# Kernel optimization log

Measured on AMD Instinct MI355X. Metric: run time of the kernel, lower is better.

The kernel has to match this reference:

```python
import jax, jax.numpy as jnp
import numpy as np

EPS = 1e-6
SIGMA = 0.02  # inverse-quadratic kernel scale (RGBuvHistBlock default)
H_BINS = 128


def _rgb_uv_hist(x, mu):
    # x: [B, 3, H, W] in [0, 1]; mu: [h] bin centers in [-3, 3]
    x = jnp.clip(x, 0.0, 1.0)
    B = x.shape[0]
    I = x.reshape(B, 3, -1)                       # [B, 3, N]
    Iy = jnp.sqrt(jnp.sum(I * I, axis=1) + EPS)   # [B, N] intensity scaling
    logI = jnp.log(I + EPS)                       # [B, 3, N]

    def kern(d):
        # inverse-quadratic kernel: 1 / (1 + (|d| / sigma)^2)
        return 1.0 / (1.0 + (d / SIGMA) ** 2)

    def chan(c0, c1, c2):
        Iu = logI[:, c0] - logI[:, c1]            # [B, N]
        Iv = logI[:, c0] - logI[:, c2]            # [B, N]
        du = kern(jnp.abs(Iu[:, :, None] - mu[None, None, :]))  # [B, N, h]
        dv = kern(jnp.abs(Iv[:, :, None] - mu[None, None, :]))  # [B, N, h]
        a = Iy[:, :, None] * du                   # [B, N, h]
        return jnp.einsum('bnu,bnv->buv', a, dv)  # [B, h, h]

    # channel order: r vs (g,b), g vs (r,b), b vs (r,g)
    hists = jnp.stack([chan(0, 1, 2), chan(1, 0, 2), chan(2, 0, 1)], axis=1)  # [B,3,h,h]
    norm = jnp.sum(hists, axis=(1, 2, 3)).reshape(-1, 1, 1, 1) + EPS
    return hists / norm


def setup_inputs() -> dict:
    key = jax.random.key(0)
    k1, k2 = jax.random.split(key)
    B, C, H, W = 4, 3, 256, 256
    pred = jax.random.uniform(k1, (B, C, H, W), dtype=jnp.float32)
    target = jax.random.uniform(k2, (B, C, H, W), dtype=jnp.float32)
    return {"pred": pred, "target": target}


def reference(pred, target):
    mu = jnp.linspace(-3.0, 3.0, H_BINS, dtype=pred.dtype)
    pred_hist = _rgb_uv_hist(pred, mu)
    target_hist = _rgb_uv_hist(target, mu)
    diff = jnp.sqrt(target_hist) - jnp.sqrt(pred_hist)
    return (1.0 / np.sqrt(2.0)) * jnp.sqrt(jnp.sum(diff * diff)) / pred_hist.shape[0]
```

## Files before the change

kernel.cpp:

```cpp
#include <hip/hip_runtime.h>

#define NPIX   65536
#define HB     128
#define EPSF   1e-6f
#define ROWB   80
#define MATB   (HB * ROWB)
#define BUFB   (3 * MATB)
#define PPW    24576

typedef _Float16 half8  __attribute__((ext_vector_type(8)));
typedef __fp16   fp16x2 __attribute__((ext_vector_type(2)));
typedef float    f32x16 __attribute__((ext_vector_type(16)));
typedef float    f32x2  __attribute__((ext_vector_type(2)));

__device__ __forceinline__ unsigned pk2(float a, float b) {
    union { fp16x2 h; unsigned u; } cv;
    cv.h = __builtin_amdgcn_cvt_pkrtz(a, b);
    return cv.u;
}

__global__ __launch_bounds__(256, 2) void hist_mfma(
    const float* __restrict__ pred, const float* __restrict__ tgt,
    unsigned* __restrict__ parts, float* __restrict__ norms, int nchunk)
{
    __shared__ char smat[2 * BUFB];

    const int t    = threadIdx.x;
    const int lane = t & 63;
    const int wave = t >> 6;
    const int chunk = blockIdx.x % nchunk;
    const int ib    = blockIdx.x / nchunk;
    const int b     = ib & 3;
    const int img   = ib >> 2;
    const int kchunk = NPIX / nchunk;
    const int nreg   = kchunk >> 5;

    const float* __restrict__ base = (img ? tgt : pred) + (size_t)b * 3 * NPIX;
    const float* __restrict__ Rp = base;
    const float* __restrict__ Gp = base + NPIX;
    const float* __restrict__ Bp = base + 2 * NPIX;

    const int   i16     = lane & 15;
    const int   r4      = lane >> 4;
    const int   rowbase = wave * 4 + r4;
    const float MU0     = (float)rowbase * (300.0f / 127.0f) - 150.0f;
    const float MUSTEP  = 16.0f * (300.0f / 127.0f);
    char* genp0 = smat + rowbase * ROWB + i16 * 4;
    char* genp1 = genp0 + BUFB;

    const int ti2 = wave >> 1;
    const int tj2 = wave & 1;

    f32x16 acc[3][2][2];
#pragma unroll
    for (int g = 0; g < 3; ++g)
#pragma unroll
        for (int i = 0; i < 2; ++i)
#pragma unroll
            for (int j = 0; j < 2; ++j)
#pragma unroll
                for (int r = 0; r < 16; ++r) acc[g][i][j][r] = 0.0f;

    const int n0 = chunk * kchunk;

    f32x2 Ra, Ga, Ba, Rb, Gb, Bb;
    f32x2 ddrg, ddrb, ddgb, rw2;

    auto issue_ld = [&](int reg, f32x2& R, f32x2& G, f32x2& B) {
        const int n = n0 + reg * 32 + 2 * i16;
        R = *reinterpret_cast<const f32x2*>(Rp + n);
        G = *reinterpret_cast<const f32x2*>(Gp + n);
        B = *reinterpret_cast<const f32x2*>(Bp + n);
    };

    auto scalars = [&](f32x2 R, f32x2 G, f32x2 B) {
        const float C = 34.65735902799726547086f;
        float r0 = fminf(fmaxf(R.x, 0.0f), 1.0f);
        float r1 = fminf(fmaxf(R.y, 0.0f), 1.0f);
        float g0 = fminf(fmaxf(G.x, 0.0f), 1.0f);
        float g1 = fminf(fmaxf(G.y, 0.0f), 1.0f);
        float b0 = fminf(fmaxf(B.x, 0.0f), 1.0f);
        float b1 = fminf(fmaxf(B.y, 0.0f), 1.0f);
        float lr0 = __builtin_amdgcn_logf(r0 + EPSF);
        float lr1 = __builtin_amdgcn_logf(r1 + EPSF);
        float lg0 = __builtin_amdgcn_logf(g0 + EPSF);
        float lg1 = __builtin_amdgcn_logf(g1 + EPSF);
        float lb0 = __builtin_amdgcn_logf(b0 + EPSF);
        float lb1 = __builtin_amdgcn_logf(b1 + EPSF);
        ddrg.x = (lr0 - lg0) * C;  ddrg.y = (lr1 - lg1) * C;
        ddrb.x = (lr0 - lb0) * C;  ddrb.y = (lr1 - lb1) * C;
        ddgb.x = (lg0 - lb0) * C;  ddgb.y = (lg1 - lb1) * C;
        const float s0 = __builtin_fmaf(r0, r0,
                          __builtin_fmaf(g0, g0,
                           __builtin_fmaf(b0, b0, EPSF)));
        const float s1 = __builtin_fmaf(r1, r1,
                          __builtin_fmaf(g1, g1,
                           __builtin_fmaf(b1, b1, EPSF)));
        rw2.x = __builtin_amdgcn_sqrtf(__builtin_amdgcn_sqrtf(s0));
        rw2.y = __builtin_amdgcn_sqrtf(__builtin_amdgcn_sqrtf(s1));
    };

    auto gen_mat = [&](char* bp, int mat, f32x2 dd) {
        float m = MU0;
#pragma unroll
        for (int s = 0; s < 8; ++s) {
            const float ex = dd.x - m, ey = dd.y - m;
            const float tx = __builtin_fmaf(ex, ex, 1.0f);
            const float ty = __builtin_fmaf(ey, ey, 1.0f);
            const float vx = __builtin_amdgcn_rcpf(tx) * rw2.x;
            const float vy = __builtin_amdgcn_rcpf(ty) * rw2.y;
            *reinterpret_cast<unsigned*>(bp + mat * MATB + s * 16 * ROWB)
                = pk2(vx, vy);
            m += MUSTEP;
        }
    };

    auto rd = [&](const char* mp, int matid, int row, int koff) -> half8 {
        return *reinterpret_cast<const half8*>(mp + matid * MATB
                                               + row * ROWB + koff);
    };

    auto body = [&](const char* mp, char* gp, bool dogen) {
        const int kbase = (lane >> 5) << 4;
        const int r0 = ti2 * 64 + (lane & 31);
        const int c0 = tj2 * 64 + (lane & 31);

        if (dogen) gen_mat(gp, 0, ddrg);
        {
            half8 a0 = rd(mp, 0, r0,      kbase);
            half8 a1 = rd(mp, 0, r0 + 32, kbase);
            half8 p0 = rd(mp, 1, c0,      kbase);
            half8 p1 = rd(mp, 1, c0 + 32, kbase);
            __builtin_amdgcn_s_setprio(1);
            acc[0][0][0] = __builtin_amdgcn_mfma_f32_32x32x16_f16(a0, p0, acc[0][0][0], 0, 0, 0);
            acc[0][0][1] = __builtin_amdgcn_mfma_f32_32x32x16_f16(a0, p1, acc[0][0][1], 0, 0, 0);
            acc[0][1][0] = __builtin_amdgcn_mfma_f32_32x32x16_f16(a1, p0, acc[0][1][0], 0, 0, 0);
            acc[0][1][1] = __builtin_amdgcn_mfma_f32_32x32x16_f16(a1, p1, acc[0][1][1], 0, 0, 0);
            __builtin_amdgcn_s_setprio(0);

            if (dogen) gen_mat(gp, 1, ddrb);
            half8 q0  = rd(mp, 2, c0,      kbase);
            half8 q1  = rd(mp, 2, c0 + 32, kbase);
            half8 bb0 = rd(mp, 1, r0,      kbase);
            half8 bb1 = rd(mp, 1, r0 + 32, kbase);
            __builtin_amdgcn_s_setprio(1);
            acc[1][0][0] = __builtin_amdgcn_mfma_f32_32x32x16_f16(a0, q0, acc[1][0][0], 0, 0, 0);
            acc[1][0][1] = __builtin_amdgcn_mfma_f32_32x32x16_f16(a0, q1, acc[1][0][1], 0, 0, 0);
            acc[1][1][0] = __builtin_amdgcn_mfma_f32_32x32x16_f16(a1, q0, acc[1][1][0], 0, 0, 0);
            acc[1][1][1] = __builtin_amdgcn_mfma_f32_32x32x16_f16(a1, q1, acc[1][1][1], 0, 0, 0);
            acc[2][0][0] = __builtin_amdgcn_mfma_f32_32x32x16_f16(bb0, q0, acc[2][0][0], 0, 0, 0);
            acc[2][0][1] = __builtin_amdgcn_mfma_f32_32x32x16_f16(bb0, q1, acc[2][0][1], 0, 0, 0);
            acc[2][1][0] = __builtin_amdgcn_mfma_f32_32x32x16_f16(bb1, q0, acc[2][1][0], 0, 0, 0);
            acc[2][1][1] = __builtin_amdgcn_mfma_f32_32x32x16_f16(bb1, q1, acc[2][1][1], 0, 0, 0);
            __builtin_amdgcn_s_setprio(0);
        }

        if (dogen) gen_mat(gp, 2, ddgb);
        {
            const int k1 = 32 + kbase;
            half8 a0  = rd(mp, 0, r0,      k1);
            half8 a1  = rd(mp, 0, r0 + 32, k1);
            half8 p0  = rd(mp, 1, c0,      k1);
            half8 p1  = rd(mp, 1, c0 + 32, k1);
            half8 q0  = rd(mp, 2, c0,      k1);
            half8 q1  = rd(mp, 2, c0 + 32, k1);
            half8 bb0 = rd(mp, 1, r0,      k1);
            half8 bb1 = rd(mp, 1, r0 + 32, k1);
            __builtin_amdgcn_s_setprio(1);
            acc[0][0][0] = __builtin_amdgcn_mfma_f32_32x32x16_f16(a0, p0, acc[0][0][0], 0, 0, 0);
            acc[0][0][1] = __builtin_amdgcn_mfma_f32_32x32x16_f16(a0, p1, acc[0][0][1], 0, 0, 0);
            acc[0][1][0] = __builtin_amdgcn_mfma_f32_32x32x16_f16(a1, p0, acc[0][1][0], 0, 0, 0);
            acc[0][1][1] = __builtin_amdgcn_mfma_f32_32x32x16_f16(a1, p1, acc[0][1][1], 0, 0, 0);
            acc[1][0][0] = __builtin_amdgcn_mfma_f32_32x32x16_f16(a0, q0, acc[1][0][0], 0, 0, 0);
            acc[1][0][1] = __builtin_amdgcn_mfma_f32_32x32x16_f16(a0, q1, acc[1][0][1], 0, 0, 0);
            acc[1][1][0] = __builtin_amdgcn_mfma_f32_32x32x16_f16(a1, q0, acc[1][1][0], 0, 0, 0);
            acc[1][1][1] = __builtin_amdgcn_mfma_f32_32x32x16_f16(a1, q1, acc[1][1][1], 0, 0, 0);
            acc[2][0][0] = __builtin_amdgcn_mfma_f32_32x32x16_f16(bb0, q0, acc[2][0][0], 0, 0, 0);
            acc[2][0][1] = __builtin_amdgcn_mfma_f32_32x32x16_f16(bb0, q1, acc[2][0][1], 0, 0, 0);
            acc[2][1][0] = __builtin_amdgcn_mfma_f32_32x32x16_f16(bb1, q0, acc[2][1][0], 0, 0, 0);
            acc[2][1][1] = __builtin_amdgcn_mfma_f32_32x32x16_f16(bb1, q1, acc[2][1][1], 0, 0, 0);
            __builtin_amdgcn_s_setprio(0);
        }
    };

    issue_ld(0, Ra, Ga, Ba);
    scalars(Ra, Ga, Ba);
    gen_mat(genp0, 0, ddrg);
    gen_mat(genp0, 1, ddrb);
    gen_mat(genp0, 2, ddgb);
    issue_ld(1, Rb, Gb, Bb);
    __syncthreads();

    for (int rg = 0; rg < nreg; rg += 2) {
        scalars(Rb, Gb, Bb);
        issue_ld(min(rg + 2, nreg - 1), Ra, Ga, Ba);
        body(smat, genp1, true);
        __syncthreads();
        scalars(Ra, Ga, Ba);
        issue_ld(min(rg + 3, nreg - 1), Rb, Gb, Bb);
        body(smat + BUFB, genp0, rg + 2 < nreg);
        __syncthreads();
    }

    unsigned* pb0 = parts + (size_t)blockIdx.x * PPW;
    float blksum = 0.0f;
#pragma unroll
    for (int g = 0; g < 3; ++g)
#pragma unroll
        for (int i2 = 0; i2 < 2; ++i2)
#pragma unroll
            for (int j2 = 0; j2 < 2; ++j2) {
                unsigned* wp = pb0
                    + (size_t)((((g * 4 + wave) * 2 + i2) * 2 + j2) * 8) * 64
                    + lane;
#pragma unroll
                for (int rh = 0; rh < 8; ++rh) {
                    wp[rh * 64] = pk2(acc[g][i2][j2][2 * rh],
                                      acc[g][i2][j2][2 * rh + 1]);
                    blksum += acc[g][i2][j2][2 * rh]
                            + acc[g][i2][j2][2 * rh + 1];
                }
            }

    for (int o = 32; o > 0; o >>= 1) blksum += __shfl_down(blksum, o, 64);
    __shared__ float wsum[4];
    if (lane == 0) wsum[wave] = blksum;
    __syncthreads();
    if (t == 0)
        atomicAdd(&norms[ib], wsum[0] + wsum[1] + wsum[2] + wsum[3]);
}

__global__ __launch_bounds__(256) void reduce_loss(
    const unsigned* __restrict__ parts, const float* __restrict__ norms,
    float* __restrict__ acc, int nchunk)
{
    const int i      = blockIdx.x * 256 + threadIdx.x;
    const int comb12 = i >> 13;
    const int rest   = i & 8191;
    const int b      = comb12 / 3;
    const int g      = comb12 % 3;
    const unsigned* pp = parts + (size_t)(b * nchunk) * PPW + g * 8192 + rest;
    const unsigned* pt = parts + (size_t)((4 + b) * nchunk) * PPW + g * 8192 + rest;

    float hp0 = 0.0f, hp1 = 0.0f, ht0 = 0.0f, ht1 = 0.0f;
    int k = 0;
    for (; k + 8 <= nchunk; k += 8) {
#pragma unroll
        for (int j = 0; j < 8; ++j) {
            union { unsigned u; fp16x2 h; } a, c;
            a.u = pp[(size_t)(k + j) * PPW];
            c.u = pt[(size_t)(k + j) * PPW];
            hp0 += (float)a.h.x;  hp1 += (float)a.h.y;
            ht0 += (float)c.h.x;  ht1 += (float)c.h.y;
        }
    }
    for (; k < nchunk; ++k) {
        union { unsigned u; fp16x2 h; } a, c;
        a.u = pp[(size_t)k * PPW];
        c.u = pt[(size_t)k * PPW];
        hp0 += (float)a.h.x;  hp1 += (float)a.h.y;
        ht0 += (float)c.h.x;  ht1 += (float)c.h.y;
    }

    const float rp = __builtin_amdgcn_rcpf(norms[b] + EPSF);
    const float rt = __builtin_amdgcn_rcpf(norms[4 + b] + EPSF);
    const float d0 = __builtin_amdgcn_sqrtf(ht0 * rt)
                   - __builtin_amdgcn_sqrtf(hp0 * rp);
    const float d1 = __builtin_amdgcn_sqrtf(ht1 * rt)
                   - __builtin_amdgcn_sqrtf(hp1 * rp);
    float s = __builtin_fmaf(d0, d0, d1 * d1);
    for (int o = 32; o > 0; o >>= 1) s += __shfl_down(s, o, 64);
    __shared__ float wsum[4];
    if ((threadIdx.x & 63) == 0) wsum[threadIdx.x >> 6] = s;
    __syncthreads();
    if (threadIdx.x == 0) atomicAdd(acc, wsum[0] + wsum[1] + wsum[2] + wsum[3]);
}

__global__ void final_k(const float* __restrict__ acc, float* __restrict__ out)
{
    out[0] = __builtin_amdgcn_sqrtf(acc[0]) * 0.70710678118654752440f * 0.25f;
}

extern "C" void kernel_launch(void* const* d_in, const int* in_sizes, int n_in,
                              void* d_out, int out_size, void* d_ws, size_t ws_size,
                              hipStream_t stream)
{
    const float* pred = (const float*)d_in[0];
    const float* tgt  = (const float*)d_in[1];
    float* ws  = (float*)d_ws;
    float* out = (float*)d_out;

    float*    norms = ws;
    float*    acc   = ws + 8;
    unsigned* parts = (unsigned*)(ws + 16);

    int nchunk = 64;
    while (nchunk > 1) {
        const size_t need = (16 + (size_t)8 * nchunk * PPW) * sizeof(float);
        if (need <= ws_size) break;
        nchunk >>= 1;
    }

    (void)hipMemsetAsync(ws, 0, 9 * sizeof(float), stream);

    hist_mfma<<<8 * nchunk, 256, 0, stream>>>(pred, tgt, parts, norms, nchunk);
    reduce_loss<<<12 * 8192 / 256, 256, 0, stream>>>(parts, norms, acc, nchunk);
    final_k<<<1, 1, 0, stream>>>(acc, out);
}
```

Baseline: 99.46 us.

## Use 512-thread blocks with 8 waves and halve histogram chunk count

Each histogram block now has 8 waves instead of 4. Each wave owns a 64x32 output tile instead of 64x64, and the per-thread basis-matrix generation is split across twice as many threads. The pixel chunk count is cut from 64 to 32, so each block handles more pixels and writes half as many fp16 partial histograms, which shrinks the reduce_loss read volume and the partial-write traffic. In exchange, each wave issues more LDS operand reads per MFMA and has fewer accumulators to overlap, and there are fewer blocks per CU.

```diff
diff --git a/kernel.cpp b/kernel.cpp
--- a/kernel.cpp
+++ b/kernel.cpp
@@ -7,6 +7,7 @@
 #define MATB   (HB * ROWB)
 #define BUFB   (3 * MATB)
 #define PPW    24576
+#define NCHUNK 32
 
 typedef _Float16 half8  __attribute__((ext_vector_type(8)));
 typedef __fp16   fp16x2 __attribute__((ext_vector_type(2)));
@@ -19,11 +20,12 @@
     return cv.u;
 }
 
-__global__ __launch_bounds__(256, 2) void hist_mfma(
+__global__ __launch_bounds__(512, 2) void hist_mfma(
     const float* __restrict__ pred, const float* __restrict__ tgt,
     unsigned* __restrict__ parts, float* __restrict__ norms, int nchunk)
 {
     __shared__ char smat[2 * BUFB];
+    __shared__ float wsum[8];
 
     const int t    = threadIdx.x;
     const int lane = t & 63;
@@ -40,26 +42,24 @@
     const float* __restrict__ Gp = base + NPIX;
     const float* __restrict__ Bp = base + 2 * NPIX;
 
-    const int   i16     = lane & 15;
-    const int   r4      = lane >> 4;
-    const int   rowbase = wave * 4 + r4;
-    const float MU0     = (float)rowbase * (300.0f / 127.0f) - 150.0f;
-    const float MUSTEP  = 16.0f * (300.0f / 127.0f);
-    char* genp0 = smat + rowbase * ROWB + i16 * 4;
+    const int   i16     = t & 15;
+    const int   rbase   = t >> 4;
+    const float MU0     = (float)rbase * (300.0f / 127.0f) - 150.0f;
+    const float MUSTEP  = 32.0f * (300.0f / 127.0f);
+    char* genp0 = smat + rbase * ROWB + i16 * 4;
     char* genp1 = genp0 + BUFB;
 
-    const int ti2 = wave >> 1;
-    const int tj2 = wave & 1;
-
-    f32x16 acc[3][2][2];
+    const int wu = wave >> 2;
+    const int wv = wave & 3;
+    const int la = lane & 31;
+
+    f32x16 acc[3][2];
 #pragma unroll
     for (int g = 0; g < 3; ++g)
 #pragma unroll
         for (int i = 0; i < 2; ++i)
 #pragma unroll
-            for (int j = 0; j < 2; ++j)
-#pragma unroll
-                for (int r = 0; r < 16; ++r) acc[g][i][j][r] = 0.0f;
+            for (int r = 0; r < 16; ++r) acc[g][i][r] = 0.0f;
 
     const int n0 = chunk * kchunk;
 
@@ -103,13 +103,13 @@
     auto gen_mat = [&](char* bp, int mat, f32x2 dd) {
         float m = MU0;
 #pragma unroll
-        for (int s = 0; s < 8; ++s) {
+        for (int s = 0; s < 4; ++s) {
             const float ex = dd.x - m, ey = dd.y - m;
             const float tx = __builtin_fmaf(ex, ex, 1.0f);
             const float ty = __builtin_fmaf(ey, ey, 1.0f);
             const float vx = __builtin_amdgcn_rcpf(tx) * rw2.x;
             const float vy = __builtin_amdgcn_rcpf(ty) * rw2.y;
-            *reinterpret_cast<unsigned*>(bp + mat * MATB + s * 16 * ROWB)
+            *reinterpret_cast<unsigned*>(bp + mat * MATB + s * 32 * ROWB)
                 = pk2(vx, vy);
             m += MUSTEP;
         }
@@ -122,36 +122,28 @@
 
     auto body = [&](const char* mp, char* gp, bool dogen) {
         const int kbase = (lane >> 5) << 4;
-        const int r0 = ti2 * 64 + (lane & 31);
-        const int c0 = tj2 * 64 + (lane & 31);
+        const int r0 = wu * 64 + la;
+        const int c0 = wv * 32 + la;
 
         if (dogen) gen_mat(gp, 0, ddrg);
         {
             half8 a0 = rd(mp, 0, r0,      kbase);
             half8 a1 = rd(mp, 0, r0 + 32, kbase);
-            half8 p0 = rd(mp, 1, c0,      kbase);
-            half8 p1 = rd(mp, 1, c0 + 32, kbase);
+            half8 p  = rd(mp, 1, c0,      kbase);
             __builtin_amdgcn_s_setprio(1);
-            acc[0][0][0] = __builtin_amdgcn_mfma_f32_32x32x16_f16(a0, p0, acc[0][0][0], 0, 0, 0);
-            acc[0][0][1] = __builtin_amdgcn_mfma_f32_32x32x16_f16(a0, p1, acc[0][0][1], 0, 0, 0);
-            acc[0][1][0] = __builtin_amdgcn_mfma_f32_32x32x16_f16(a1, p0, acc[0][1][0], 0, 0, 0);
-            acc[0][1][1] = __builtin_amdgcn_mfma_f32_32x32x16_f16(a1, p1, acc[0][1][1], 0, 0, 0);
+            acc[0][0] = __builtin_amdgcn_mfma_f32_32x32x16_f16(a0, p, acc[0][0], 0, 0, 0);
+            acc[0][1] = __builtin_amdgcn_mfma_f32_32x32x16_f16(a1, p, acc[0][1], 0, 0, 0);
             __builtin_amdgcn_s_setprio(0);
 
             if (dogen) gen_mat(gp, 1, ddrb);
-            half8 q0  = rd(mp, 2, c0,      kbase);
-            half8 q1  = rd(mp, 2, c0 + 32, kbase);
+            half8 q   = rd(mp, 2, c0,      kbase);
             half8 bb0 = rd(mp, 1, r0,      kbase);
             half8 bb1 = rd(mp, 1, r0 + 32, kbase);
             __builtin_amdgcn_s_setprio(1);
-            acc[1][0][0] = __builtin_amdgcn_mfma_f32_32x32x16_f16(a0, q0, acc[1][0][0], 0, 0, 0);
-            acc[1][0][1] = __builtin_amdgcn_mfma_f32_32x32x16_f16(a0, q1, acc[1][0][1], 0, 0, 0);
-            acc[1][1][0] = __builtin_amdgcn_mfma_f32_32x32x16_f16(a1, q0, acc[1][1][0], 0, 0, 0);
-            acc[1][1][1] = __builtin_amdgcn_mfma_f32_32x32x16_f16(a1, q1, acc[1][1][1], 0, 0, 0);
-            acc[2][0][0] = __builtin_amdgcn_mfma_f32_32x32x16_f16(bb0, q0, acc[2][0][0], 0, 0, 0);
-            acc[2][0][1] = __builtin_amdgcn_mfma_f32_32x32x16_f16(bb0, q1, acc[2][0][1], 0, 0, 0);
-            acc[2][1][0] = __builtin_amdgcn_mfma_f32_32x32x16_f16(bb1, q0, acc[2][1][0], 0, 0, 0);
-            acc[2][1][1] = __builtin_amdgcn_mfma_f32_32x32x16_f16(bb1, q1, acc[2][1][1], 0, 0, 0);
+            acc[1][0] = __builtin_amdgcn_mfma_f32_32x32x16_f16(a0, q, acc[1][0], 0, 0, 0);
+            acc[1][1] = __builtin_amdgcn_mfma_f32_32x32x16_f16(a1, q, acc[1][1], 0, 0, 0);
+            acc[2][0] = __builtin_amdgcn_mfma_f32_32x32x16_f16(bb0, q, acc[2][0], 0, 0, 0);
+            acc[2][1] = __builtin_amdgcn_mfma_f32_32x32x16_f16(bb1, q, acc[2][1], 0, 0, 0);
             __builtin_amdgcn_s_setprio(0);
         }
 
@@ -160,25 +152,17 @@
             const int k1 = 32 + kbase;
             half8 a0  = rd(mp, 0, r0,      k1);
             half8 a1  = rd(mp, 0, r0 + 32, k1);
-            half8 p0  = rd(mp, 1, c0,      k1);
-            half8 p1  = rd(mp, 1, c0 + 32, k1);
-            half8 q0  = rd(mp, 2, c0,      k1);
-            half8 q1  = rd(mp, 2, c0 + 32, k1);
+            half8 p   = rd(mp, 1, c0,      k1);
+            half8 q   = rd(mp, 2, c0,      k1);
             half8 bb0 = rd(mp, 1, r0,      k1);
             half8 bb1 = rd(mp, 1, r0 + 32, k1);
             __builtin_amdgcn_s_setprio(1);
-            acc[0][0][0] = __builtin_amdgcn_mfma_f32_32x32x16_f16(a0, p0, acc[0][0][0], 0, 0, 0);
-            acc[0][0][1] = __builtin_amdgcn_mfma_f32_32x32x16_f16(a0, p1, acc[0][0][1], 0, 0, 0);
-            acc[0][1][0] = __builtin_amdgcn_mfma_f32_32x32x16_f16(a1, p0, acc[0][1][0], 0, 0, 0);
-            acc[0][1][1] = __builtin_amdgcn_mfma_f32_32x32x16_f16(a1, p1, acc[0][1][1], 0, 0, 0);
-            acc[1][0][0] = __builtin_amdgcn_mfma_f32_32x32x16_f16(a0, q0, acc[1][0][0], 0, 0, 0);
-            acc[1][0][1] = __builtin_amdgcn_mfma_f32_32x32x16_f16(a0, q1, acc[1][0][1], 0, 0, 0);
-            acc[1][1][0] = __builtin_amdgcn_mfma_f32_32x32x16_f16(a1, q0, acc[1][1][0], 0, 0, 0);
-            acc[1][1][1] = __builtin_amdgcn_mfma_f32_32x32x16_f16(a1, q1, acc[1][1][1], 0, 0, 0);
-            acc[2][0][0] = __builtin_amdgcn_mfma_f32_32x32x16_f16(bb0, q0, acc[2][0][0], 0, 0, 0);
-            acc[2][0][1] = __builtin_amdgcn_mfma_f32_32x32x16_f16(bb0, q1, acc[2][0][1], 0, 0, 0);
-            acc[2][1][0] = __builtin_amdgcn_mfma_f32_32x32x16_f16(bb1, q0, acc[2][1][0], 0, 0, 0);
-            acc[2][1][1] = __builtin_amdgcn_mfma_f32_32x32x16_f16(bb1, q1, acc[2][1][1], 0, 0, 0);
+            acc[0][0] = __builtin_amdgcn_mfma_f32_32x32x16_f16(a0, p, acc[0][0], 0, 0, 0);
+            acc[0][1] = __builtin_amdgcn_mfma_f32_32x32x16_f16(a1, p, acc[0][1], 0, 0, 0);
+            acc[1][0] = __builtin_amdgcn_mfma_f32_32x32x16_f16(a0, q, acc[1][0], 0, 0, 0);
+            acc[1][1] = __builtin_amdgcn_mfma_f32_32x32x16_f16(a1, q, acc[1][1], 0, 0, 0);
+            acc[2][0] = __builtin_amdgcn_mfma_f32_32x32x16_f16(bb0, q, acc[2][0], 0, 0, 0);
+            acc[2][1] = __builtin_amdgcn_mfma_f32_32x32x16_f16(bb1, q, acc[2][1], 0, 0, 0);
             __builtin_amdgcn_s_setprio(0);
         }
     };
@@ -207,27 +191,25 @@
 #pragma unroll
     for (int g = 0; g < 3; ++g)
 #pragma unroll
-        for (int i2 = 0; i2 < 2; ++i2)
-#pragma unroll
-            for (int j2 = 0; j2 < 2; ++j2) {
-                unsigned* wp = pb0
-                    + (size_t)((((g * 4 + wave) * 2 + i2) * 2 + j2) * 8) * 64
-                    + lane;
-#pragma unroll
-                for (int rh = 0; rh < 8; ++rh) {
-                    wp[rh * 64] = pk2(acc[g][i2][j2][2 * rh],
-                                      acc[g][i2][j2][2 * rh + 1]);
-                    blksum += acc[g][i2][j2][2 * rh]
-                            + acc[g][i2][j2][2 * rh + 1];
-                }
+        for (int i2 = 0; i2 < 2; ++i2) {
+            unsigned* wp = pb0
+                + (size_t)(((g * 8 + wave) * 2 + i2) * 8) * 64 + lane;
+#pragma unroll
+            for (int rh = 0; rh < 8; ++rh) {
+                wp[rh * 64] = pk2(acc[g][i2][2 * rh], acc[g][i2][2 * rh + 1]);
+                blksum += acc[g][i2][2 * rh] + acc[g][i2][2 * rh + 1];
             }
+        }
 
     for (int o = 32; o > 0; o >>= 1) blksum += __shfl_down(blksum, o, 64);
-    __shared__ float wsum[4];
     if (lane == 0) wsum[wave] = blksum;
     __syncthreads();
-    if (t == 0)
-        atomicAdd(&norms[ib], wsum[0] + wsum[1] + wsum[2] + wsum[3]);
+    if (t == 0) {
+        float s = 0.0f;
+#pragma unroll
+        for (int w = 0; w < 8; ++w) s += wsum[w];
+        atomicAdd(&norms[ib], s);
+    }
 }
 
 __global__ __launch_bounds__(256) void reduce_loss(
@@ -294,7 +276,7 @@
     float*    acc   = ws + 8;
     unsigned* parts = (unsigned*)(ws + 16);
 
-    int nchunk = 64;
+    int nchunk = NCHUNK;
     while (nchunk > 1) {
         const size_t need = (16 + (size_t)8 * nchunk * PPW) * sizeof(float);
         if (need <= ws_size) break;
@@ -303,7 +285,7 @@
 
     (void)hipMemsetAsync(ws, 0, 9 * sizeof(float), stream);
 
-    hist_mfma<<<8 * nchunk, 256, 0, stream>>>(pred, tgt, parts, norms, nchunk);
+    hist_mfma<<<8 * nchunk, 512, 0, stream>>>(pred, tgt, parts, norms, nchunk);
     reduce_loss<<<12 * 8192 / 256, 256, 0, stream>>>(parts, norms, acc, nchunk);
     final_k<<<1, 1, 0, stream>>>(acc, out);
 }
```

Result: no change. 100.9 us (+1.4%).

## Gather pixels via DPP for 16-byte LDS stores and fold final kernel into reduction

Applied to the files above, without the earlier changes.

The kernel-matrix generation now has each lane compute four pixels' values for one bin row. It gathers the neighbouring lanes' log-differences and weights with quad-permute DPP moves, then writes a 16-byte uint4 to LDS instead of eight scattered 4-byte stores. This reduces LDS store instruction count and bank traffic at the cost of extra DPP moves and registers. Separately, the final sqrt kernel is removed: the last reduce_loss block, detected with an atomic counter, writes the output. This saves one kernel launch but adds a fence and an atomic per block.

```diff
diff --git a/kernel.cpp b/kernel.cpp
--- a/kernel.cpp
+++ b/kernel.cpp
@@ -19,11 +19,22 @@
     return cv.u;
 }
 
+#define QPF(x, c) __int_as_float(__builtin_amdgcn_mov_dpp(                  \
+                      __float_as_int(x), (c), 0xf, 0xf, true))
+#define GATHER4(dst, src)                                                   \
+    do {                                                                    \
+        dst[0].x = QPF(src.x, 0x00); dst[0].y = QPF(src.y, 0x00);           \
+        dst[1].x = QPF(src.x, 0x55); dst[1].y = QPF(src.y, 0x55);           \
+        dst[2].x = QPF(src.x, 0xAA); dst[2].y = QPF(src.y, 0xAA);           \
+        dst[3].x = QPF(src.x, 0xFF); dst[3].y = QPF(src.y, 0xFF);           \
+    } while (0)
+
 __global__ __launch_bounds__(256, 2) void hist_mfma(
     const float* __restrict__ pred, const float* __restrict__ tgt,
     unsigned* __restrict__ parts, float* __restrict__ norms, int nchunk)
 {
     __shared__ char smat[2 * BUFB];
+    __shared__ float wsumS[4];
 
     const int t    = threadIdx.x;
     const int lane = t & 63;
@@ -41,11 +52,13 @@
     const float* __restrict__ Bp = base + 2 * NPIX;
 
     const int   i16     = lane & 15;
-    const int   r4      = lane >> 4;
-    const int   rowbase = wave * 4 + r4;
-    const float MU0     = (float)rowbase * (300.0f / 127.0f) - 150.0f;
-    const float MUSTEP  = 16.0f * (300.0f / 127.0f);
-    char* genp0 = smat + rowbase * ROWB + i16 * 4;
+    const int   rowslot = (lane & 3) + 4 * (lane >> 4);
+    const int   pxgrp   = (lane >> 2) & 3;
+    const int   rb0     = rowslot + 16 * wave;
+    const float STEP    = 300.0f / 127.0f;
+    const float MU0     = (float)rb0 * STEP - 150.0f;
+    const float MU64    = 64.0f * STEP;
+    char* genp0 = smat + rb0 * ROWB + pxgrp * 16;
     char* genp1 = genp0 + BUFB;
 
     const int ti2 = wave >> 1;
@@ -65,6 +78,7 @@
 
     f32x2 Ra, Ga, Ba, Rb, Gb, Bb;
     f32x2 ddrg, ddrb, ddgb, rw2;
+    f32x2 rwq[4];
 
     auto issue_ld = [&](int reg, f32x2& R, f32x2& G, f32x2& B) {
         const int n = n0 + reg * 32 + 2 * i16;
@@ -98,20 +112,27 @@
                            __builtin_fmaf(b1, b1, EPSF)));
         rw2.x = __builtin_amdgcn_sqrtf(__builtin_amdgcn_sqrtf(s0));
         rw2.y = __builtin_amdgcn_sqrtf(__builtin_amdgcn_sqrtf(s1));
-    };
-
-    auto gen_mat = [&](char* bp, int mat, f32x2 dd) {
-        float m = MU0;
-#pragma unroll
-        for (int s = 0; s < 8; ++s) {
-            const float ex = dd.x - m, ey = dd.y - m;
-            const float tx = __builtin_fmaf(ex, ex, 1.0f);
-            const float ty = __builtin_fmaf(ey, ey, 1.0f);
-            const float vx = __builtin_amdgcn_rcpf(tx) * rw2.x;
-            const float vy = __builtin_amdgcn_rcpf(ty) * rw2.y;
-            *reinterpret_cast<unsigned*>(bp + mat * MATB + s * 16 * ROWB)
-                = pk2(vx, vy);
-            m += MUSTEP;
+        GATHER4(rwq, rw2);
+    };
+
+    auto gen_mat = [&](char* gp, int mat, f32x2 dd) {
+        f32x2 dq[4];
+        GATHER4(dq, dd);
+#pragma unroll
+        for (int s = 0; s < 2; ++s) {
+            const float m = MU0 + (s ? MU64 : 0.0f);
+            unsigned w[4];
+#pragma unroll
+            for (int q = 0; q < 4; ++q) {
+                const float ex = dq[q].x - m, ey = dq[q].y - m;
+                const float vx = __builtin_amdgcn_rcpf(
+                                     __builtin_fmaf(ex, ex, 1.0f)) * rwq[q].x;
+                const float vy = __builtin_amdgcn_rcpf(
+                                     __builtin_fmaf(ey, ey, 1.0f)) * rwq[q].y;
+                w[q] = pk2(vx, vy);
+            }
+            uint4 qv; qv.x = w[0]; qv.y = w[1]; qv.z = w[2]; qv.w = w[3];
+            *reinterpret_cast<uint4*>(gp + mat * MATB + s * 64 * ROWB) = qv;
         }
     };
 
@@ -223,16 +244,16 @@
             }
 
     for (int o = 32; o > 0; o >>= 1) blksum += __shfl_down(blksum, o, 64);
-    __shared__ float wsum[4];
-    if (lane == 0) wsum[wave] = blksum;
+    if (lane == 0) wsumS[wave] = blksum;
     __syncthreads();
     if (t == 0)
-        atomicAdd(&norms[ib], wsum[0] + wsum[1] + wsum[2] + wsum[3]);
+        atomicAdd(&norms[ib], wsumS[0] + wsumS[1] + wsumS[2] + wsumS[3]);
 }
 
 __global__ __launch_bounds__(256) void reduce_loss(
     const unsigned* __restrict__ parts, const float* __restrict__ norms,
-    float* __restrict__ acc, int nchunk)
+    float* __restrict__ acc, unsigned* __restrict__ cnt,
+    float* __restrict__ out, int nchunk)
 {
     const int i      = blockIdx.x * 256 + threadIdx.x;
     const int comb12 = i >> 13;
@@ -273,12 +294,16 @@
     __shared__ float wsum[4];
     if ((threadIdx.x & 63) == 0) wsum[threadIdx.x >> 6] = s;
     __syncthreads();
-    if (threadIdx.x == 0) atomicAdd(acc, wsum[0] + wsum[1] + wsum[2] + wsum[3]);
-}
-
-__global__ void final_k(const float* __restrict__ acc, float* __restrict__ out)
-{
-    out[0] = __builtin_amdgcn_sqrtf(acc[0]) * 0.70710678118654752440f * 0.25f;
+    if (threadIdx.x == 0) {
+        atomicAdd(acc, wsum[0] + wsum[1] + wsum[2] + wsum[3]);
+        __threadfence();
+        const unsigned done = atomicAdd(cnt, 1u);
+        if (done == gridDim.x - 1) {
+            const float v = atomicAdd(acc, 0.0f);
+            out[0] = __builtin_amdgcn_sqrtf(v)
+                   * 0.70710678118654752440f * 0.25f;
+        }
+    }
 }
 
 extern "C" void kernel_launch(void* const* d_in, const int* in_sizes, int n_in,
@@ -292,6 +317,7 @@
 
     float*    norms = ws;
     float*    acc   = ws + 8;
+    unsigned* cnt   = (unsigned*)(ws + 9);
     unsigned* parts = (unsigned*)(ws + 16);
 
     int nchunk = 64;
@@ -301,9 +327,9 @@
         nchunk >>= 1;
     }
 
-    (void)hipMemsetAsync(ws, 0, 9 * sizeof(float), stream);
+    (void)hipMemsetAsync(ws, 0, 16 * sizeof(float), stream);
 
     hist_mfma<<<8 * nchunk, 256, 0, stream>>>(pred, tgt, parts, norms, nchunk);
-    reduce_loss<<<12 * 8192 / 256, 256, 0, stream>>>(parts, norms, acc, nchunk);
-    final_k<<<1, 1, 0, stream>>>(acc, out);
+    reduce_loss<<<12 * 8192 / 256, 256, 0, stream>>>(parts, norms, acc, cnt,
+                                                     out, nchunk);
 }
```

New measurement: 111.6 us. +12.2%, slower.
